# Performance work log

Measured on AMD Instinct MI355X. Metric: run time of the kernel, lower is better.

The kernel has to match this reference:

```python
import jax, jax.numpy as jnp
import numpy as np

N_NODES = 100000
N_EDGES = 1200000
N_GRAPHS = 512


def _init_linear(key, fan_in, fan_out):
    kw, kb = jax.random.split(key)
    lim = 1.0 / np.sqrt(fan_in)
    W = jax.random.uniform(kw, (fan_in, fan_out), minval=-lim, maxval=lim, dtype=jnp.float32)
    b = jax.random.uniform(kb, (fan_out,), minval=-lim, maxval=lim, dtype=jnp.float32)
    return W, b


def setup_inputs() -> dict:
    key = jax.random.key(0)
    ks = jax.random.split(key, 12)
    x = jax.random.normal(ks[0], (N_NODES, 10), dtype=jnp.float32)
    edge_index = jax.random.randint(ks[1], (2, N_EDGES), 0, N_NODES, dtype=jnp.int64)
    batch = jnp.sort(jax.random.randint(ks[2], (N_NODES,), 0, N_GRAPHS, dtype=jnp.int64))
    edge_weights = jax.random.uniform(ks[3], (N_EDGES,), dtype=jnp.float32)
    W1, b1 = _init_linear(ks[4], 10, 60)
    W2, b2 = _init_linear(ks[5], 60, 60)
    W3, b3 = _init_linear(ks[6], 60, 60)
    W4, b4 = _init_linear(ks[7], 60, 60)
    L1w, L1b = _init_linear(ks[8], 60, 60)
    L2w, L2b = _init_linear(ks[9], 60, 10)
    L3w, L3b = _init_linear(ks[10], 10, 2)
    return dict(x=x, edge_index=edge_index, batch=batch, edge_weights=edge_weights,
                W1=W1, b1=b1, W2=W2, b2=b2, W3=W3, b3=b3, W4=W4, b4=b4,
                L1w=L1w, L1b=L1b, L2w=L2w, L2b=L2b, L3w=L3w, L3b=L3b)


def gcn_conv(x, W, b, src, dst, ew, n):
    # PyG GCNConv: add self-loops (weight 1), symmetric normalization, linear, scatter-add.
    deg = jax.ops.segment_sum(ew, dst, num_segments=n) + 1.0  # +1 self-loop
    dinv = jnp.where(deg > 0, jax.lax.rsqrt(deg), 0.0)
    h = x @ W  # [n, out]
    norm = dinv[src] * ew * dinv[dst]  # [E]
    agg = jax.ops.segment_sum(h[src] * norm[:, None], dst, num_segments=n)
    agg = agg + h * (dinv * dinv)[:, None]  # self-loop contribution (weight 1)
    return agg + b


def _forward(x, edge_index, batch, edge_weights,
             W1, b1, W2, b2, W3, b3, W4, b4,
             L1w, L1b, L2w, L2b, L3w, L3b):
    src, dst = edge_index[0], edge_index[1]
    n = x.shape[0]
    h = jax.nn.relu(gcn_conv(x, W1, b1, src, dst, edge_weights, n))
    h = jax.nn.relu(gcn_conv(h, W2, b2, src, dst, edge_weights, n))
    h = jax.nn.relu(gcn_conv(h, W3, b3, src, dst, edge_weights, n))
    h = jax.nn.relu(gcn_conv(h, W4, b4, src, dst, edge_weights, n))
    g = jax.ops.segment_max(h, batch, num_segments=N_GRAPHS)
    g = jnp.where(jnp.isfinite(g), g, 0.0)  # guard empty graphs
    g = jax.nn.relu(g @ L1w + L1b)
    g = jax.nn.relu(g @ L2w + L2b)
    return g @ L3w + L3b


def reference(x, edge_index, batch, edge_weights,
              W1, b1, W2, b2, W3, b3, W4, b4,
              L1w, L1b, L2w, L2b, L3w, L3b):
    return _forward(x, edge_index, batch, edge_weights,
                    W1, b1, W2, b2, W3, b3, W4, b4,
                    L1w, L1b, L2w, L2b, L3w, L3b)
```

## Files before the change

kernel.cpp:

```cpp
#include <hip/hip_runtime.h>
#include <hip/hip_fp16.h>

#define N_NODES 100000
#define N_EDGES 1200000
#define N_GRAPHS 512
#define F 60
#define NPW 8
#define CAP 48
#define GSTRIDE 384
#define NBKT 782
#define EPB 4096
#define CPX 37
#define NCH 296
#define BKT_CAP 2048
#define WSC 3.0518509e-05f

__global__ void __launch_bounds__(256) k_hist(const int* __restrict__ dst,
                                              int* __restrict__ histM, int E) {
    __shared__ int h[NBKT];
    int c = (blockIdx.x & 7) * CPX + (blockIdx.x >> 3);
    for (int i = threadIdx.x; i < NBKT; i += 256) h[i] = 0;
    __syncthreads();
    int b0 = c * EPB;
    for (int i = threadIdx.x; i < EPB; i += 256) {
        int e = b0 + i;
        if (e < E) atomicAdd(&h[dst[e] >> 7], 1);
    }
    __syncthreads();
    for (int i = threadIdx.x; i < NBKT; i += 256) histM[c * NBKT + i] = h[i];
}

__global__ void k_scan_gstart(int* __restrict__ histM, int* __restrict__ tot,
                              const int* __restrict__ batch, int* __restrict__ gst, int n) {
    int bi = blockIdx.x;
    if (bi < 4) {
        int b = bi * 256 + threadIdx.x;
        if (b >= NBKT) return;
        int running = 0;
        for (int c = 0; c < NCH; c += 8) {
            int i0 = (c + 0) * NBKT + b, i1 = (c + 1) * NBKT + b;
            int i2 = (c + 2) * NBKT + b, i3 = (c + 3) * NBKT + b;
            int i4 = (c + 4) * NBKT + b, i5 = (c + 5) * NBKT + b;
            int i6 = (c + 6) * NBKT + b, i7 = (c + 7) * NBKT + b;
            int v0 = histM[i0], v1 = histM[i1], v2 = histM[i2], v3 = histM[i3];
            int v4 = histM[i4], v5 = histM[i5], v6 = histM[i6], v7 = histM[i7];
            histM[i0] = running; running += v0;
            histM[i1] = running; running += v1;
            histM[i2] = running; running += v2;
            histM[i3] = running; running += v3;
            histM[i4] = running; running += v4;
            histM[i5] = running; running += v5;
            histM[i6] = running; running += v6;
            histM[i7] = running; running += v7;
        }
        tot[b] = running;
    } else {
        int i = (bi - 4) * 256 + threadIdx.x;
        if (i >= n) return;
        int b = batch[i];
        int pb = (i == 0) ? -1 : batch[i - 1];
        for (int g = pb + 1; g <= b; ++g) gst[g] = i;
        if (i == n - 1) for (int g = b + 1; g <= N_GRAPHS; ++g) gst[g] = n;
    }
}

__global__ void __launch_bounds__(256) k_fill(const int* __restrict__ src,
                                              const int* __restrict__ dst,
                                              const float* __restrict__ ew,
                                              const int* __restrict__ histM,
                                              int2* __restrict__ bkt, int E) {
    __shared__ int h[NBKT];
    int c = (blockIdx.x & 7) * CPX + (blockIdx.x >> 3);
    for (int i = threadIdx.x; i < NBKT; i += 256) h[i] = 0;
    __syncthreads();
    int b0 = c * EPB;
    const int* bas = histM + c * NBKT;
    for (int i = threadIdx.x; i < EPB; i += 256) {
        int e = b0 + i;
        if (e >= E) continue;
        int d = dst[e];
        int b = d >> 7;
        int r = atomicAdd(&h[b], 1);
        int pos = bas[b] + r;
        if (pos < BKT_CAP) {
            int2 p;
            p.x = src[e] | ((d & 127) << 17);
            p.y = __float_as_int(ew[e]);
            bkt[(size_t)b * BKT_CAP + pos] = p;
        }
    }
}

__global__ void __launch_bounds__(256) k_build(
        const int* __restrict__ tot, const int2* __restrict__ bkt,
        unsigned* __restrict__ csr, int* __restrict__ rnd,
        float* __restrict__ dinv, const float* __restrict__ x,
        float* __restrict__ xs, int n) {
    __shared__ int lcur[128];
    __shared__ float ldeg[128];
    int b = blockIdx.x, tid = threadIdx.x;
    if (tid < 128) { lcur[tid] = 0; ldeg[tid] = 0.f; }
    __syncthreads();
    int nbase = b << 7;
    int m = min(tot[b], BKT_CAP);
    const int2* sb = bkt + (size_t)b * BKT_CAP;
    for (int i = tid; i < m; i += 256) {
        int2 p = sb[i];
        int srcv = p.x & 0x1FFFF;
        int low = (p.x >> 17) & 127;
        int pos = atomicAdd(&lcur[low], 1);
        if (pos < CAP) {
            unsigned w15 = (unsigned)(int)rintf(__int_as_float(p.y) * 32767.f);
            int v = nbase + low;
            size_t idx = (size_t)(v >> 3) * GSTRIDE + (pos >> 2) * 32 + (v & 7) * 4 + (pos & 3);
            csr[idx] = (unsigned)srcv | (w15 << 17);
        }
        atomicAdd(&ldeg[low], __int_as_float(p.y));
    }
    __syncthreads();
    if (tid < 128) {
        int v = nbase + tid;
        if (v < n) {
            int mA = min(lcur[tid], CAP);
            float di = rsqrtf(ldeg[tid] + 1.0f);
            dinv[v] = di;
            #pragma unroll
            for (int c2 = 0; c2 < 10; ++c2) xs[v * 16 + c2] = di * x[v * 10 + c2];
            #pragma unroll
            for (int c2 = 10; c2 < 16; ++c2) xs[v * 16 + c2] = 0.f;
            int g0 = tid & ~7;
            int m8 = 0;
            #pragma unroll
            for (int i2 = 0; i2 < 8; ++i2) m8 = max(m8, min(lcur[g0 + i2], CAP));
            int R = (m8 + 3) & ~3;
            size_t gb = (size_t)(v >> 3) * GSTRIDE;
            int p8 = v & 7;
            for (int e = mA; e < R; ++e)
                csr[gb + (e >> 2) * 32 + p8 * 4 + (e & 3)] = 0u;
            if ((tid & 7) == 0) rnd[v >> 3] = R;
        }
    }
}

template<bool FIRST, bool SCALE_OUT>
__global__ void __launch_bounds__(256) k_layer(
        const void* __restrict__ HinV, const float* __restrict__ W,
        const float* __restrict__ bias,
        const unsigned* __restrict__ csr, const int* __restrict__ rnd,
        const float* __restrict__ dinv,
        __half* __restrict__ Hout, int n) {
    constexpr int WIN = FIRST ? 10 : 60;
    constexpr int WINP = FIRST ? 12 : 60;
    const float*  Hf = (const float*)HinV;
    const __half* Hh = (const __half*)HinV;
    __shared__ float Ws[WINP * 64];
    __shared__ __align__(16) float accS[4][NPW][64];
    for (int i = threadIdx.x; i < WINP * 64; i += 256) {
        int k = i >> 6, j = i & 63;
        Ws[i] = (j < F && k < WIN) ? W[k * F + j] : 0.f;
    }

    int wave = threadIdx.x >> 6;
    int lane = threadIdx.x & 63;
    float bj = (lane < F) ? bias[lane] : 0.f;
    int base = (blockIdx.x * 4 + wave) * NPW;
    int g = base >> 3;
    const unsigned* segG = csr + (size_t)g * GSTRIDE;
    int mu = rnd[g];

    if constexpr (FIRST) {
        __syncthreads();
        int l16 = lane & 15;
        int qt = lane >> 4;
        float a0 = Hf[(base + qt) * 16 + l16];
        float a1 = Hf[(base + 4 + qt) * 16 + l16];
        for (int e = 0; e < mu; e += 4) {
            const unsigned* ch = segG + (e >> 2) * 32;
            uint4 qa = *(const uint4*)(ch + qt * 4);
            uint4 qb = *(const uint4*)(ch + (4 + qt) * 4);
            float x0 = Hf[(qa.x & 0x1FFFF) * 16 + l16];
            float x1 = Hf[(qa.y & 0x1FFFF) * 16 + l16];
            float x2 = Hf[(qa.z & 0x1FFFF) * 16 + l16];
            float x3 = Hf[(qa.w & 0x1FFFF) * 16 + l16];
            float y0 = Hf[(qb.x & 0x1FFFF) * 16 + l16];
            float y1 = Hf[(qb.y & 0x1FFFF) * 16 + l16];
            float y2 = Hf[(qb.z & 0x1FFFF) * 16 + l16];
            float y3 = Hf[(qb.w & 0x1FFFF) * 16 + l16];
            a0 = fmaf((float)(qa.x >> 17) * WSC, x0, a0);
            a0 = fmaf((float)(qa.y >> 17) * WSC, x1, a0);
            a0 = fmaf((float)(qa.z >> 17) * WSC, x2, a0);
            a0 = fmaf((float)(qa.w >> 17) * WSC, x3, a0);
            a1 = fmaf((float)(qb.x >> 17) * WSC, y0, a1);
            a1 = fmaf((float)(qb.y >> 17) * WSC, y1, a1);
            a1 = fmaf((float)(qb.z >> 17) * WSC, y2, a1);
            a1 = fmaf((float)(qb.w >> 17) * WSC, y3, a1);
        }
        accS[wave][qt][l16]     = a0 * dinv[base + qt];
        accS[wave][4 + qt][l16] = a1 * dinv[base + 4 + qt];
        float o[NPW];
        #pragma unroll
        for (int t = 0; t < NPW; ++t) o[t] = bj;
        const float4* aq = (const float4*)&accS[wave][0][0];
        #pragma unroll
        for (int kq = 0; kq < 3; ++kq) {
            float w0 = Ws[(4 * kq + 0) * 64 + lane];
            float w1 = Ws[(4 * kq + 1) * 64 + lane];
            float w2 = Ws[(4 * kq + 2) * 64 + lane];
            float w3 = Ws[(4 * kq + 3) * 64 + lane];
            #pragma unroll
            for (int t = 0; t < NPW; ++t) {
                float4 aa = aq[t * 16 + kq];
                o[t] = fmaf(aa.x, w0, o[t]);
                o[t] = fmaf(aa.y, w1, o[t]);
                o[t] = fmaf(aa.z, w2, o[t]);
                o[t] = fmaf(aa.w, w3, o[t]);
            }
        }
        #pragma unroll
        for (int t = 0; t < NPW; ++t) {
            float sc = SCALE_OUT ? dinv[base + t] : 1.f;
            Hout[(size_t)(base + t) * 64 + lane] = __float2half_rn(fmaxf(o[t], 0.f) * sc);
        }
    } else {
        __syncthreads();
        int h  = lane >> 5;
        int lh = lane & 31;
        int fo = lh * 2;

        float2 acc2[4];
        float dis[4];
        #pragma unroll
        for (int p = 0; p < 4; ++p) {
            int v = base + 2 * p + h;
            dis[p] = dinv[v];
            __half2 sh = *(const __half2*)(Hh + (size_t)v * 64 + fo);
            acc2[p].x = __low2float(sh);
            acc2[p].y = __high2float(sh);
        }

        for (int e = 0; e < mu; e += 4) {
            const unsigned* ch = segG + (e >> 2) * 32;
            uint4 q[4];
            #pragma unroll
            for (int p = 0; p < 4; ++p) q[p] = *(const uint4*)(ch + (2 * p + h) * 4);
            #pragma unroll
            for (int p = 0; p < 4; ++p) {
                unsigned e0 = q[p].x, e1 = q[p].y, e2 = q[p].z, e3 = q[p].w;
                __half2 g0 = *(const __half2*)(Hh + (size_t)(e0 & 0x1FFFF) * 64 + fo);
                __half2 g1 = *(const __half2*)(Hh + (size_t)(e1 & 0x1FFFF) * 64 + fo);
                __half2 g2 = *(const __half2*)(Hh + (size_t)(e2 & 0x1FFFF) * 64 + fo);
                __half2 g3 = *(const __half2*)(Hh + (size_t)(e3 & 0x1FFFF) * 64 + fo);
                float w0 = (float)(e0 >> 17) * WSC;
                float w1 = (float)(e1 >> 17) * WSC;
                float w2 = (float)(e2 >> 17) * WSC;
                float w3 = (float)(e3 >> 17) * WSC;
                acc2[p].x = fmaf(w0, __low2float(g0), acc2[p].x);
                acc2[p].y = fmaf(w0, __high2float(g0), acc2[p].y);
                acc2[p].x = fmaf(w1, __low2float(g1), acc2[p].x);
                acc2[p].y = fmaf(w1, __high2float(g1), acc2[p].y);
                acc2[p].x = fmaf(w2, __low2float(g2), acc2[p].x);
                acc2[p].y = fmaf(w2, __high2float(g2), acc2[p].y);
                acc2[p].x = fmaf(w3, __low2float(g3), acc2[p].x);
                acc2[p].y = fmaf(w3, __high2float(g3), acc2[p].y);
            }
        }
        #pragma unroll
        for (int p = 0; p < 4; ++p) {
            acc2[p].x *= dis[p]; acc2[p].y *= dis[p];
            *(float2*)&accS[wave][2 * p + h][fo] = acc2[p];
        }

        float o[NPW];
        #pragma unroll
        for (int t = 0; t < NPW; ++t) o[t] = bj;
        const float4* aq = (const float4*)&accS[wave][0][0];
        #pragma unroll
        for (int kq = 0; kq < 15; ++kq) {
            float w0 = Ws[(4 * kq + 0) * 64 + lane];
            float w1 = Ws[(4 * kq + 1) * 64 + lane];
            float w2 = Ws[(4 * kq + 2) * 64 + lane];
            float w3 = Ws[(4 * kq + 3) * 64 + lane];
            #pragma unroll
            for (int t = 0; t < NPW; ++t) {
                float4 aa = aq[t * 16 + kq];
                o[t] = fmaf(aa.x, w0, o[t]);
                o[t] = fmaf(aa.y, w1, o[t]);
                o[t] = fmaf(aa.z, w2, o[t]);
                o[t] = fmaf(aa.w, w3, o[t]);
            }
        }
        #pragma unroll
        for (int t = 0; t < NPW; ++t) {
            float sc = SCALE_OUT ? dinv[base + t] : 1.f;
            Hout[(size_t)(base + t) * 64 + lane] = __float2half_rn(fmaxf(o[t], 0.f) * sc);
        }
    }
}

__global__ void __launch_bounds__(256) k_poolmlp(
        const __half* __restrict__ H, const int* __restrict__ start,
        const float* __restrict__ L1w, const float* __restrict__ L1b,
        const float* __restrict__ L2w, const float* __restrict__ L2b,
        const float* __restrict__ L3w, const float* __restrict__ L3b,
        float* __restrict__ out) {
    __shared__ float red[4 * F];
    __shared__ float gin[F], h1[F], h2[10];
    int gi = blockIdx.x;
    int wave = threadIdx.x >> 6;
    int lane = threadIdx.x & 63;
    int t = threadIdx.x;
    int s = start[gi], e = start[gi + 1];
    float m = 0.f;
    for (int i = s + wave; i < e; i += 4)
        m = fmaxf(m, __half2float(H[(size_t)i * 64 + lane]));
    if (lane < F) red[wave * F + lane] = m;
    __syncthreads();
    if (t < F)
        gin[t] = fmaxf(fmaxf(red[t], red[F + t]), fmaxf(red[2 * F + t], red[3 * F + t]));
    __syncthreads();
    if (t < F) {
        float a = L1b[t];
        for (int k = 0; k < F; ++k) a += gin[k] * L1w[k * F + t];
        h1[t] = fmaxf(a, 0.f);
    }
    __syncthreads();
    if (t < 10) {
        float a = L2b[t];
        for (int k = 0; k < F; ++k) a += h1[k] * L2w[k * 10 + t];
        h2[t] = fmaxf(a, 0.f);
    }
    __syncthreads();
    if (t < 2) {
        float a = L3b[t];
        for (int k = 0; k < 10; ++k) a += h2[k] * L3w[k * 2 + t];
        out[gi * 2 + t] = a;
    }
}

extern "C" void kernel_launch(void* const* d_in, const int* in_sizes, int n_in,
                              void* d_out, int out_size, void* d_ws, size_t ws_size,
                              hipStream_t stream) {
    const int n = N_NODES, E = N_EDGES;
    const float* x   = (const float*)d_in[0];
    const int* ei    = (const int*)d_in[1];
    const int* batch = (const int*)d_in[2];
    const float* ew  = (const float*)d_in[3];
    const float* W1 = (const float*)d_in[4],  *b1 = (const float*)d_in[5];
    const float* W2 = (const float*)d_in[6],  *b2 = (const float*)d_in[7];
    const float* W3 = (const float*)d_in[8],  *b3 = (const float*)d_in[9];
    const float* W4 = (const float*)d_in[10], *b4 = (const float*)d_in[11];
    const float* L1w = (const float*)d_in[12], *L1b = (const float*)d_in[13];
    const float* L2w = (const float*)d_in[14], *L2b = (const float*)d_in[15];
    const float* L3w = (const float*)d_in[16], *L3b = (const float*)d_in[17];
    float* out = (float*)d_out;

    const int* src = ei;
    const int* dst = ei + E;

    char* ws = (char*)d_ws;
    size_t off = 0;
    auto carve = [&](size_t bytes) {
        void* p = ws + off;
        off += (bytes + 255) & ~size_t(255);
        return p;
    };
    int*      rnd   = (int*)carve((n / 8) * 4);
    float*    dinv  = (float*)carve(n * 4);
    int*      gst   = (int*)carve((N_GRAPHS + 1) * 4);
    unsigned* csr   = (unsigned*)carve((size_t)n * CAP * 4);
    int2*     bkt   = (int2*)carve((size_t)NBKT * BKT_CAP * 8);
    int*      histM = (int*)carve((size_t)NCH * NBKT * 4);
    int*      tot   = (int*)carve(NBKT * 4);
    float*    xs    = (float*)carve((size_t)n * 16 * 4);
    __half*   hA    = (__half*)carve((size_t)n * 64 * 2);
    __half*   hB    = (__half*)carve((size_t)n * 64 * 2);
    (void)ws_size;

    const int NB = (n + 255) / 256;
    const int LB = n / (4 * NPW);

    k_hist<<<NCH, 256, 0, stream>>>(dst, histM, E);
    k_scan_gstart<<<4 + NB, 256, 0, stream>>>(histM, tot, batch, gst, n);
    k_fill<<<NCH, 256, 0, stream>>>(src, dst, ew, histM, bkt, E);
    k_build<<<NBKT, 256, 0, stream>>>(tot, bkt, csr, rnd, dinv, x, xs, n);

    k_layer<true,  true ><<<LB, 256, 0, stream>>>(xs, W1, b1, csr, rnd, dinv, hA, n);
    k_layer<false, true ><<<LB, 256, 0, stream>>>(hA, W2, b2, csr, rnd, dinv, hB, n);
    k_layer<false, true ><<<LB, 256, 0, stream>>>(hB, W3, b3, csr, rnd, dinv, hA, n);
    k_layer<false, false><<<LB, 256, 0, stream>>>(hA, W4, b4, csr, rnd, dinv, hB, n);

    k_poolmlp<<<N_GRAPHS, 256, 0, stream>>>(hB, gst, L1w, L1b, L2w, L2b, L3w, L3b, out);
}
```

Baseline: 223.1 us.

## Renumber nodes by degree within 128-node buckets to balance 8-node groups

Adds a prep kernel that counting-sorts the nodes of each 128-node bucket by clipped in-degree and assigns them permuted indices. The CSR, dinv, scaled inputs and layer outputs are stored in that permuted order, and source indices are remapped, so each 8-node group holds nodes of similar degree and pads fewer slots to the group maximum. The cost is an extra pass over the buckets, a random permidx lookup per edge during the build, and an indirect lookup during pooling.

```diff
diff --git a/kernel.cpp b/kernel.cpp
--- a/kernel.cpp
+++ b/kernel.cpp
@@ -13,6 +13,7 @@
 #define CPX 37
 #define NCH 296
 #define BKT_CAP 2048
+#define NDEG 49
 #define WSC 3.0518509e-05f
 
 __global__ void __launch_bounds__(256) k_hist(const int* __restrict__ dst,
@@ -91,17 +92,81 @@
     }
 }
 
-__global__ void __launch_bounds__(256) k_build(
+__global__ void __launch_bounds__(256) k_prep(
         const int* __restrict__ tot, const int2* __restrict__ bkt,
-        unsigned* __restrict__ csr, int* __restrict__ rnd,
-        float* __restrict__ dinv, const float* __restrict__ x,
-        float* __restrict__ xs, int n) {
+        const float* __restrict__ x,
+        int* __restrict__ permidx, float* __restrict__ dinvN,
+        float* __restrict__ xs, int* __restrict__ rnd,
+        unsigned* __restrict__ csr, int n) {
+    __shared__ int lc[128];
+    __shared__ float ld[128];
+    __shared__ int dh[NDEG];
+    __shared__ int gmax[16];
+    int b = blockIdx.x, tid = threadIdx.x;
+    if (tid < 128) { lc[tid] = 0; ld[tid] = 0.f; }
+    if (tid < NDEG) dh[tid] = 0;
+    if (tid < 16) gmax[tid] = 0;
+    __syncthreads();
+    int m = min(tot[b], BKT_CAP);
+    const int2* sb = bkt + (size_t)b * BKT_CAP;
+    for (int i = tid; i < m; i += 256) {
+        int2 p = sb[i];
+        int low = (p.x >> 17) & 127;
+        atomicAdd(&lc[low], 1);
+        atomicAdd(&ld[low], __int_as_float(p.y));
+    }
+    __syncthreads();
+    int nbase = b << 7;
+    int nvalid = min(128, n - nbase);
+    int c = 0;
+    if (tid < nvalid) { c = min(lc[tid], CAP); atomicAdd(&dh[c], 1); }
+    __syncthreads();
+    if (tid == 0) {
+        int run = 0;
+        for (int d = 0; d < NDEG; ++d) { int t = dh[d]; dh[d] = run; run += t; }
+    }
+    __syncthreads();
+    if (tid < nvalid) {
+        int r = atomicAdd(&dh[c], 1);
+        int ni = nbase + r;
+        int v = nbase + tid;
+        permidx[v] = ni;
+        float di = rsqrtf(ld[tid] + 1.0f);
+        dinvN[ni] = di;
+        #pragma unroll
+        for (int c2 = 0; c2 < 10; ++c2) xs[ni * 16 + c2] = di * x[v * 10 + c2];
+        #pragma unroll
+        for (int c2 = 10; c2 < 16; ++c2) xs[ni * 16 + c2] = 0.f;
+        atomicMax(&gmax[r >> 3], c);
+        lc[tid] = (r << 8) | c;
+    }
+    __syncthreads();
+    if (tid < 16 && (tid << 3) < nvalid)
+        rnd[(b << 4) + tid] = (gmax[tid] + 3) & ~3;
+    if (tid < nvalid) {
+        int rc = lc[tid];
+        int r = rc >> 8, c2 = rc & 255;
+        int R = (gmax[r >> 3] + 3) & ~3;
+        int ni = nbase + r;
+        size_t gb = (size_t)(ni >> 3) * GSTRIDE;
+        int p8 = ni & 7;
+        for (int e = c2; e < R; ++e)
+            csr[gb + (e >> 2) * 32 + p8 * 4 + (e & 3)] = 0u;
+    }
+}
+
+__global__ void __launch_bounds__(256) k_build2(
+        const int* __restrict__ tot, const int2* __restrict__ bkt,
+        const int* __restrict__ permidx, unsigned* __restrict__ csr, int n) {
     __shared__ int lcur[128];
-    __shared__ float ldeg[128];
+    __shared__ int pix[128];
     int b = blockIdx.x, tid = threadIdx.x;
-    if (tid < 128) { lcur[tid] = 0; ldeg[tid] = 0.f; }
-    __syncthreads();
-    int nbase = b << 7;
+    if (tid < 128) {
+        lcur[tid] = 0;
+        int v = (b << 7) + tid;
+        pix[tid] = (v < n) ? permidx[v] : 0;
+    }
+    __syncthreads();
     int m = min(tot[b], BKT_CAP);
     const int2* sb = bkt + (size_t)b * BKT_CAP;
     for (int i = tid; i < m; i += 256) {
@@ -111,33 +176,10 @@
         int pos = atomicAdd(&lcur[low], 1);
         if (pos < CAP) {
             unsigned w15 = (unsigned)(int)rintf(__int_as_float(p.y) * 32767.f);
-            int v = nbase + low;
-            size_t idx = (size_t)(v >> 3) * GSTRIDE + (pos >> 2) * 32 + (v & 7) * 4 + (pos & 3);
-            csr[idx] = (unsigned)srcv | (w15 << 17);
-        }
-        atomicAdd(&ldeg[low], __int_as_float(p.y));
-    }
-    __syncthreads();
-    if (tid < 128) {
-        int v = nbase + tid;
-        if (v < n) {
-            int mA = min(lcur[tid], CAP);
-            float di = rsqrtf(ldeg[tid] + 1.0f);
-            dinv[v] = di;
-            #pragma unroll
-            for (int c2 = 0; c2 < 10; ++c2) xs[v * 16 + c2] = di * x[v * 10 + c2];
-            #pragma unroll
-            for (int c2 = 10; c2 < 16; ++c2) xs[v * 16 + c2] = 0.f;
-            int g0 = tid & ~7;
-            int m8 = 0;
-            #pragma unroll
-            for (int i2 = 0; i2 < 8; ++i2) m8 = max(m8, min(lcur[g0 + i2], CAP));
-            int R = (m8 + 3) & ~3;
-            size_t gb = (size_t)(v >> 3) * GSTRIDE;
-            int p8 = v & 7;
-            for (int e = mA; e < R; ++e)
-                csr[gb + (e >> 2) * 32 + p8 * 4 + (e & 3)] = 0u;
-            if ((tid & 7) == 0) rnd[v >> 3] = R;
+            int ni = pix[low];
+            unsigned srcN = (unsigned)permidx[srcv];
+            size_t idx = (size_t)(ni >> 3) * GSTRIDE + (pos >> 2) * 32 + (ni & 7) * 4 + (pos & 3);
+            csr[idx] = srcN | (w15 << 17);
         }
     }
 }
@@ -299,6 +341,7 @@
 
 __global__ void __launch_bounds__(256) k_poolmlp(
         const __half* __restrict__ H, const int* __restrict__ start,
+        const int* __restrict__ permidx,
         const float* __restrict__ L1w, const float* __restrict__ L1b,
         const float* __restrict__ L2w, const float* __restrict__ L2b,
         const float* __restrict__ L3w, const float* __restrict__ L3b,
@@ -311,8 +354,10 @@
     int t = threadIdx.x;
     int s = start[gi], e = start[gi + 1];
     float m = 0.f;
-    for (int i = s + wave; i < e; i += 4)
-        m = fmaxf(m, __half2float(H[(size_t)i * 64 + lane]));
+    for (int i = s + wave; i < e; i += 4) {
+        int ni = permidx[i];
+        m = fmaxf(m, __half2float(H[(size_t)ni * 64 + lane]));
+    }
     if (lane < F) red[wave * F + lane] = m;
     __syncthreads();
     if (t < F)
@@ -365,7 +410,8 @@
         return p;
     };
     int*      rnd   = (int*)carve((n / 8) * 4);
-    float*    dinv  = (float*)carve(n * 4);
+    float*    dinvN = (float*)carve(n * 4);
+    int*      permidx = (int*)carve(n * 4);
     int*      gst   = (int*)carve((N_GRAPHS + 1) * 4);
     unsigned* csr   = (unsigned*)carve((size_t)n * CAP * 4);
     int2*     bkt   = (int2*)carve((size_t)NBKT * BKT_CAP * 8);
@@ -382,12 +428,14 @@
     k_hist<<<NCH, 256, 0, stream>>>(dst, histM, E);
     k_scan_gstart<<<4 + NB, 256, 0, stream>>>(histM, tot, batch, gst, n);
     k_fill<<<NCH, 256, 0, stream>>>(src, dst, ew, histM, bkt, E);
-    k_build<<<NBKT, 256, 0, stream>>>(tot, bkt, csr, rnd, dinv, x, xs, n);
-
-    k_layer<true,  true ><<<LB, 256, 0, stream>>>(xs, W1, b1, csr, rnd, dinv, hA, n);
-    k_layer<false, true ><<<LB, 256, 0, stream>>>(hA, W2, b2, csr, rnd, dinv, hB, n);
-    k_layer<false, true ><<<LB, 256, 0, stream>>>(hB, W3, b3, csr, rnd, dinv, hA, n);
-    k_layer<false, false><<<LB, 256, 0, stream>>>(hA, W4, b4, csr, rnd, dinv, hB, n);
-
-    k_poolmlp<<<N_GRAPHS, 256, 0, stream>>>(hB, gst, L1w, L1b, L2w, L2b, L3w, L3b, out);
-}
+    k_prep<<<NBKT, 256, 0, stream>>>(tot, bkt, x, permidx, dinvN, xs, rnd, csr, n);
+    k_build2<<<NBKT, 256, 0, stream>>>(tot, bkt, permidx, csr, n);
+
+    k_layer<true,  true ><<<LB, 256, 0, stream>>>(xs, W1, b1, csr, rnd, dinvN, hA, n);
+    k_layer<false, true ><<<LB, 256, 0, stream>>>(hA, W2, b2, csr, rnd, dinvN, hB, n);
+    k_layer<false, true ><<<LB, 256, 0, stream>>>(hB, W3, b3, csr, rnd, dinvN, hA, n);
+    k_layer<false, false><<<LB, 256, 0, stream>>>(hA, W4, b4, csr, rnd, dinvN, hB, n);
+
+    k_poolmlp<<<N_GRAPHS, 256, 0, stream>>>(hB, gst, permidx,
+                                            L1w, L1b, L2w, L2b, L3w, L3b, out);
+}
```

After: 240.2 us. +7.6%, slower.
